# Kernel tuning notes

Hardware: AMD Instinct MI355X
Metric: run time of the kernel (lower is better)

The kernel has to match this reference:

```python
import jax, jax.numpy as jnp
import numpy as np

NUM_FEATURES = 512
NUM_HID = 16
NUM_CLASSES = 40


def _glorot(key, shape):
    lim = float(np.sqrt(6.0 / (shape[0] + shape[1])))
    return jax.random.uniform(key, shape, jnp.float32, -lim, lim)


def setup_inputs() -> dict:
    key = jax.random.key(0)
    k1, k2, k3, k4 = jax.random.split(key, 4)
    N, E = 100000, 3200000
    x = jax.random.normal(k1, (N, NUM_FEATURES), jnp.float32)
    edge_index = jax.random.randint(k2, (2, E), 0, N, jnp.int64)
    W1 = _glorot(k3, (NUM_FEATURES, NUM_HID))
    b1 = jnp.zeros((NUM_HID,), jnp.float32)
    W2 = _glorot(k4, (NUM_HID, NUM_CLASSES))
    b2 = jnp.zeros((NUM_CLASSES,), jnp.float32)
    return {"x": x, "edge_index": edge_index, "num_nodes": N,
            "W1": W1, "b1": b1, "W2": W2, "b2": b2}


def gcn_conv(x, src, dst, norm, W, b, num_nodes):
    # linear transform first (PyG GCNConv), then normalized scatter-add
    h = x @ W                                    # [N, out]
    msg = h[src] * norm[:, None]                 # [E+N, out]
    agg = jax.ops.segment_sum(msg, dst, num_segments=num_nodes)
    return agg + b


def reference(x, edge_index, num_nodes, W1, b1, W2, b2):
    # add self-loops and compute symmetric normalization deg^-1/2 A_hat deg^-1/2
    loops = jnp.arange(num_nodes, dtype=edge_index.dtype)
    src = jnp.concatenate([edge_index[0], loops])
    dst = jnp.concatenate([edge_index[1], loops])
    ones = jnp.ones(src.shape, x.dtype)
    deg = jax.ops.segment_sum(ones, dst, num_segments=num_nodes)
    dinv = jnp.where(deg > 0, deg ** -0.5, 0.0)
    norm = dinv[src] * dinv[dst]

    h = jax.nn.relu(gcn_conv(x, src, dst, norm, W1, b1, num_nodes))
    # dropout omitted: inference mode (training=False)
    h = gcn_conv(h, src, dst, norm, W2, b2, num_nodes)
    out = jax.nn.softmax(h, axis=1)
    return (out, h)
```

## Files before the change

### kernel.cpp

```cpp
#include <hip/hip_runtime.h>
#include <math.h>

#define F 512
#define H 16
#define C 40
#define BW 128
#define BSH 7
#define NB_MAX 1024
#define CHUNK 4096
#define EPT 16
#define SRC_BITS 17
#define SRC_MASK 0x1FFFF
#define SORT_CAP 8192

__global__ __launch_bounds__(256) void k_scatfuse(const int* __restrict__ src,
                                                  const int* __restrict__ dst,
                                                  int* __restrict__ gcnt,
                                                  int* __restrict__ ebuf, int E, int NB) {
    __shared__ int hist[NB_MAX];
    __shared__ int base2[NB_MAX];
    __shared__ int cur[NB_MAX];
    __shared__ int tsum[256];
    __shared__ int paddr[CHUNK];
    __shared__ int pdata[CHUNK];
    int c = blockIdx.x, t = threadIdx.x;
    int i0 = c * CHUNK;
    int nval = min(CHUNK, E - i0);
    for (int b = t; b < NB; b += 256) hist[b] = 0;
    int dreg[EPT], sreg[EPT];
    #pragma unroll
    for (int j = 0; j < EPT; j++) {
        int i = t + j * 256;
        if (i < nval) { dreg[j] = dst[i0 + i]; sreg[j] = src[i0 + i]; }
        else dreg[j] = -1;
    }
    __syncthreads();
    #pragma unroll
    for (int j = 0; j < EPT; j++)
        if (dreg[j] >= 0) atomicAdd(&hist[dreg[j] >> BSH], 1);
    __syncthreads();
    int b0 = t * 4;
    int v0 = (b0 + 0 < NB) ? hist[b0 + 0] : 0;
    int v1 = (b0 + 1 < NB) ? hist[b0 + 1] : 0;
    int v2 = (b0 + 2 < NB) ? hist[b0 + 2] : 0;
    int v3 = (b0 + 3 < NB) ? hist[b0 + 3] : 0;
    int loc1 = v0, loc2 = v0 + v1, loc3 = v0 + v1 + v2;
    int s = loc3 + v3;
    tsum[t] = s;
    __syncthreads();
    for (int off = 1; off < 256; off <<= 1) {
        int v = (t >= off) ? tsum[t - off] : 0;
        __syncthreads();
        tsum[t] += v;
        __syncthreads();
    }
    int excl = tsum[t] - s;
    if (b0 + 0 < NB) { int p = excl;        cur[b0+0] = p; int g = v0 ? atomicAdd(&gcnt[b0+0], v0) : 0; base2[b0+0] = (b0+0)*SORT_CAP + g - p; }
    if (b0 + 1 < NB) { int p = excl + loc1; cur[b0+1] = p; int g = v1 ? atomicAdd(&gcnt[b0+1], v1) : 0; base2[b0+1] = (b0+1)*SORT_CAP + g - p; }
    if (b0 + 2 < NB) { int p = excl + loc2; cur[b0+2] = p; int g = v2 ? atomicAdd(&gcnt[b0+2], v2) : 0; base2[b0+2] = (b0+2)*SORT_CAP + g - p; }
    if (b0 + 3 < NB) { int p = excl + loc3; cur[b0+3] = p; int g = v3 ? atomicAdd(&gcnt[b0+3], v3) : 0; base2[b0+3] = (b0+3)*SORT_CAP + g - p; }
    __syncthreads();
    #pragma unroll
    for (int j = 0; j < EPT; j++) {
        int d = dreg[j];
        if (d < 0) continue;
        int b = d >> BSH;
        int r = atomicAdd(&cur[b], 1);
        paddr[r] = base2[b] + r;
        pdata[r] = ((d & (BW - 1)) << SRC_BITS) | sreg[j];
    }
    __syncthreads();
    for (int i = t; i < nval; i += 256)
        ebuf[paddr[i]] = pdata[i];
}

__global__ __launch_bounds__(256) void k_sortb(int* __restrict__ ebuf,
                                               const int* __restrict__ gcnt,
                                               int* __restrict__ rowbeg,
                                               int* __restrict__ rowend,
                                               float* __restrict__ dinv, int N) {
    __shared__ int buf[SORT_CAP];
    __shared__ int hist[BW];
    __shared__ int off[BW];
    __shared__ int cur[BW];
    int b = blockIdx.x;
    int beg = b * SORT_CAP;
    int len = gcnt[b];
    if (len > SORT_CAP) len = SORT_CAP;
    int tid = threadIdx.x;
    if (tid < BW) hist[tid] = 0;
    for (int i = tid; i < len; i += 256) buf[i] = ebuf[beg + i];
    __syncthreads();
    for (int i = tid; i < len; i += 256)
        atomicAdd(&hist[buf[i] >> SRC_BITS], 1);
    __syncthreads();
    if (tid < BW) off[tid] = hist[tid];
    __syncthreads();
    for (int d = 1; d < BW; d <<= 1) {
        int v = (tid < BW && tid >= d) ? off[tid - d] : 0;
        __syncthreads();
        if (tid < BW) off[tid] += v;
        __syncthreads();
    }
    if (tid < BW) {
        int excl = off[tid] - hist[tid];
        int n = b * BW + tid;
        if (n < N) {
            rowbeg[n] = beg + excl;
            rowend[n] = beg + off[tid];
            dinv[n] = rsqrtf((float)(hist[tid] + 1));
        }
        cur[tid] = excl;
    }
    __syncthreads();
    for (int i = tid; i < len; i += 256) {
        int w = buf[i];
        int r = atomicAdd(&cur[w >> SRC_BITS], 1);
        ebuf[beg + r] = w & SRC_MASK;
    }
}

#define KT 64
#define GST 68
__global__ __launch_bounds__(64) void k_gemm1(const float* __restrict__ x,
                                              const float* __restrict__ W1,
                                              const float* __restrict__ dinv,
                                              float* __restrict__ h0s, int N) {
    __shared__ float xs[64 * GST];
    int t = threadIdx.x;
    int n0 = blockIdx.x * 64;
    float acc[H];
    #pragma unroll
    for (int j = 0; j < H; j++) acc[j] = 0.f;
    for (int kt = 0; kt < F; kt += KT) {
        __syncthreads();
        #pragma unroll
        for (int p = 0; p < 16; p++) {
            int idx = t + (p << 6);
            int r = idx >> 4, c4 = idx & 15;
            int v = n0 + r; if (v >= N) v = N - 1;
            float4 val = *(const float4*)(x + (size_t)v * F + kt + (c4 << 2));
            *(float4*)&xs[r * GST + (c4 << 2)] = val;
        }
        __syncthreads();
        #pragma unroll
        for (int k4 = 0; k4 < 16; k4++) {
            float4 xv = *(const float4*)&xs[t * GST + (k4 << 2)];
            const float* w = W1 + (size_t)(kt + (k4 << 2)) * H;
            #pragma unroll
            for (int j = 0; j < H; j++) acc[j] = fmaf(xv.x, w[j], acc[j]);
            #pragma unroll
            for (int j = 0; j < H; j++) acc[j] = fmaf(xv.y, w[H + j], acc[j]);
            #pragma unroll
            for (int j = 0; j < H; j++) acc[j] = fmaf(xv.z, w[2 * H + j], acc[j]);
            #pragma unroll
            for (int j = 0; j < H; j++) acc[j] = fmaf(xv.w, w[3 * H + j], acc[j]);
        }
    }
    int v = n0 + t;
    if (v >= N) return;
    float dv = dinv[v];
    float4* o4 = (float4*)(h0s + (size_t)v * H);
    o4[0] = make_float4(acc[0] * dv, acc[1] * dv, acc[2] * dv, acc[3] * dv);
    o4[1] = make_float4(acc[4] * dv, acc[5] * dv, acc[6] * dv, acc[7] * dv);
    o4[2] = make_float4(acc[8] * dv, acc[9] * dv, acc[10] * dv, acc[11] * dv);
    o4[3] = make_float4(acc[12] * dv, acc[13] * dv, acc[14] * dv, acc[15] * dv);
}

__global__ __launch_bounds__(256) void k_agg1(const float* __restrict__ hs,
                                              const int* __restrict__ adj,
                                              const int* __restrict__ rowbeg,
                                              const int* __restrict__ rowend,
                                              const float* __restrict__ dinv,
                                              const float* __restrict__ b1,
                                              float* __restrict__ out, int N) {
    int t = blockIdx.x * 256 + threadIdx.x;
    int n = t >> 2, q = t & 3;
    if (n >= N) return;
    const float4* hs4 = (const float4*)hs;
    int beg = rowbeg[n], end = rowend[n];
    float4 a = hs4[(size_t)n * 4 + q];
    float ax = a.x, ay = a.y, az = a.z, aw = a.w;
    int e = beg;
    for (; e + 7 < end; e += 8) {
        int s0 = adj[e], s1 = adj[e + 1], s2 = adj[e + 2], s3 = adj[e + 3];
        int s4 = adj[e + 4], s5 = adj[e + 5], s6 = adj[e + 6], s7 = adj[e + 7];
        float4 v0 = hs4[(size_t)s0 * 4 + q];
        float4 v1 = hs4[(size_t)s1 * 4 + q];
        float4 v2 = hs4[(size_t)s2 * 4 + q];
        float4 v3 = hs4[(size_t)s3 * 4 + q];
        float4 v4 = hs4[(size_t)s4 * 4 + q];
        float4 v5 = hs4[(size_t)s5 * 4 + q];
        float4 v6 = hs4[(size_t)s6 * 4 + q];
        float4 v7 = hs4[(size_t)s7 * 4 + q];
        ax += ((v0.x + v1.x) + (v2.x + v3.x)) + ((v4.x + v5.x) + (v6.x + v7.x));
        ay += ((v0.y + v1.y) + (v2.y + v3.y)) + ((v4.y + v5.y) + (v6.y + v7.y));
        az += ((v0.z + v1.z) + (v2.z + v3.z)) + ((v4.z + v5.z) + (v6.z + v7.z));
        aw += ((v0.w + v1.w) + (v2.w + v3.w)) + ((v4.w + v5.w) + (v6.w + v7.w));
    }
    for (; e + 3 < end; e += 4) {
        int s0 = adj[e], s1 = adj[e + 1], s2 = adj[e + 2], s3 = adj[e + 3];
        float4 v0 = hs4[(size_t)s0 * 4 + q];
        float4 v1 = hs4[(size_t)s1 * 4 + q];
        float4 v2 = hs4[(size_t)s2 * 4 + q];
        float4 v3 = hs4[(size_t)s3 * 4 + q];
        ax += (v0.x + v1.x) + (v2.x + v3.x);
        ay += (v0.y + v1.y) + (v2.y + v3.y);
        az += (v0.z + v1.z) + (v2.z + v3.z);
        aw += (v0.w + v1.w) + (v2.w + v3.w);
    }
    for (; e < end; e++) {
        int s = adj[e];
        float4 v = hs4[(size_t)s * 4 + q];
        ax += v.x; ay += v.y; az += v.z; aw += v.w;
    }
    float dv = dinv[n];
    float4 r;
    r.x = fmaxf(fmaf(dv, ax, b1[q * 4 + 0]), 0.f) * dv;
    r.y = fmaxf(fmaf(dv, ay, b1[q * 4 + 1]), 0.f) * dv;
    r.z = fmaxf(fmaf(dv, az, b1[q * 4 + 2]), 0.f) * dv;
    r.w = fmaxf(fmaf(dv, aw, b1[q * 4 + 3]), 0.f) * dv;
    ((float4*)out)[(size_t)n * 4 + q] = r;
}

__global__ __launch_bounds__(256) void k_agg2out(const float* __restrict__ hs,
                                                 const int* __restrict__ adj,
                                                 const int* __restrict__ rowbeg,
                                                 const int* __restrict__ rowend,
                                                 const float* __restrict__ dinv,
                                                 const float* __restrict__ W2,
                                                 const float* __restrict__ b2,
                                                 float* __restrict__ dout, int N) {
    __shared__ float sg[64 * 16];
    __shared__ float w2s[H * C];
    __shared__ float b2s[C];
    __shared__ float so[64 * 40];
    int t = threadIdx.x;
    for (int i = t; i < H * C; i += 256) w2s[i] = W2[i];
    if (t < C) b2s[t] = b2[t];
    int nl = t >> 2, q = t & 3;
    int n0 = blockIdx.x * 64;
    int n = n0 + nl;
    bool valid = (n < N);
    int nn = valid ? n : N - 1;
    const float4* hs4 = (const float4*)hs;
    int beg = rowbeg[nn], end = rowend[nn];
    float4 a = hs4[(size_t)nn * 4 + q];
    float ax = a.x, ay = a.y, az = a.z, aw = a.w;
    int e = beg;
    for (; e + 7 < end; e += 8) {
        int s0 = adj[e], s1 = adj[e + 1], s2 = adj[e + 2], s3 = adj[e + 3];
        int s4 = adj[e + 4], s5 = adj[e + 5], s6 = adj[e + 6], s7 = adj[e + 7];
        float4 v0 = hs4[(size_t)s0 * 4 + q];
        float4 v1 = hs4[(size_t)s1 * 4 + q];
        float4 v2 = hs4[(size_t)s2 * 4 + q];
        float4 v3 = hs4[(size_t)s3 * 4 + q];
        float4 v4 = hs4[(size_t)s4 * 4 + q];
        float4 v5 = hs4[(size_t)s5 * 4 + q];
        float4 v6 = hs4[(size_t)s6 * 4 + q];
        float4 v7 = hs4[(size_t)s7 * 4 + q];
        ax += ((v0.x + v1.x) + (v2.x + v3.x)) + ((v4.x + v5.x) + (v6.x + v7.x));
        ay += ((v0.y + v1.y) + (v2.y + v3.y)) + ((v4.y + v5.y) + (v6.y + v7.y));
        az += ((v0.z + v1.z) + (v2.z + v3.z)) + ((v4.z + v5.z) + (v6.z + v7.z));
        aw += ((v0.w + v1.w) + (v2.w + v3.w)) + ((v4.w + v5.w) + (v6.w + v7.w));
    }
    for (; e + 3 < end; e += 4) {
        int s0 = adj[e], s1 = adj[e + 1], s2 = adj[e + 2], s3 = adj[e + 3];
        float4 v0 = hs4[(size_t)s0 * 4 + q];
        float4 v1 = hs4[(size_t)s1 * 4 + q];
        float4 v2 = hs4[(size_t)s2 * 4 + q];
        float4 v3 = hs4[(size_t)s3 * 4 + q];
        ax += (v0.x + v1.x) + (v2.x + v3.x);
        ay += (v0.y + v1.y) + (v2.y + v3.y);
        az += (v0.z + v1.z) + (v2.z + v3.z);
        aw += (v0.w + v1.w) + (v2.w + v3.w);
    }
    for (; e < end; e++) {
        int s = adj[e];
        float4 v = hs4[(size_t)s * 4 + q];
        ax += v.x; ay += v.y; az += v.z; aw += v.w;
    }
    float dv = dinv[nn];
    *(float4*)&sg[nl * 16 + q * 4] = make_float4(dv * ax, dv * ay, dv * az, dv * aw);
    __syncthreads();
    float g16[16];
    #pragma unroll
    for (int k4 = 0; k4 < 4; k4++) {
        float4 gv = *(const float4*)&sg[nl * 16 + k4 * 4];
        g16[k4 * 4] = gv.x; g16[k4 * 4 + 1] = gv.y;
        g16[k4 * 4 + 2] = gv.z; g16[k4 * 4 + 3] = gv.w;
    }
    int j0 = q * 10;
    float h2[10];
    #pragma unroll
    for (int jj = 0; jj < 10; jj++) {
        float acc = b2s[j0 + jj];
        #pragma unroll
        for (int k = 0; k < H; k++) acc = fmaf(g16[k], w2s[k * C + j0 + jj], acc);
        h2[jj] = acc;
    }
    float m = h2[0];
    #pragma unroll
    for (int jj = 1; jj < 10; jj++) m = fmaxf(m, h2[jj]);
    m = fmaxf(m, __shfl_xor(m, 1, 64));
    m = fmaxf(m, __shfl_xor(m, 2, 64));
    float ex[10], ssum = 0.f;
    #pragma unroll
    for (int jj = 0; jj < 10; jj++) { ex[jj] = __expf(h2[jj] - m); ssum += ex[jj]; }
    ssum += __shfl_xor(ssum, 1, 64);
    ssum += __shfl_xor(ssum, 2, 64);
    float inv = 1.f / ssum;
    int rows = min(64, N - n0);
    int tot = rows * 10;
    #pragma unroll
    for (int jj = 0; jj < 10; jj++) so[nl * 40 + j0 + jj] = ex[jj] * inv;
    __syncthreads();
    {
        const float4* sp4 = (const float4*)so;
        float4* o4 = (float4*)(dout + (size_t)n0 * C);
        for (int i = t; i < tot; i += 256) o4[i] = sp4[i];
    }
    __syncthreads();
    #pragma unroll
    for (int jj = 0; jj < 10; jj++) so[nl * 40 + j0 + jj] = h2[jj];
    __syncthreads();
    {
        const float4* sp4 = (const float4*)so;
        float4* o4 = (float4*)(dout + (size_t)N * C + (size_t)n0 * C);
        for (int i = t; i < tot; i += 256) o4[i] = sp4[i];
    }
}

extern "C" void kernel_launch(void* const* d_in, const int* in_sizes, int n_in,
                              void* d_out, int out_size, void* d_ws, size_t ws_size,
                              hipStream_t stream) {
    const float* x  = (const float*)d_in[0];
    const int*   ei = (const int*)d_in[1];
    const float* W1 = (const float*)d_in[3];
    const float* b1 = (const float*)d_in[4];
    const float* W2 = (const float*)d_in[5];
    const float* b2 = (const float*)d_in[6];
    float* out = (float*)d_out;

    int N = in_sizes[0] / F;
    int E = in_sizes[1] / 2;
    const int* src = ei;
    const int* dst = ei + E;
    int NB  = (N + BW - 1) / BW;
    int NCH = (E + CHUNK - 1) / CHUNK;

    float* ws = (float*)d_ws;
    size_t o = 0;
    int* gcnt   = (int*)(ws + o); o += (size_t)NB_MAX;
    int* rowbeg = (int*)(ws + o); o += (size_t)N + 4;
    int* rowend = (int*)(ws + o); o += (size_t)N + 4;
    int* ebuf   = (int*)(ws + o); o += (size_t)NB * SORT_CAP + CHUNK;
    float* dinv = ws + o;         o += (size_t)N;
    float* h0s  = ws + o;         o += (size_t)N * H;
    float* h1s  = ws + o;         o += (size_t)N * H;

    int ng = (N + 63) / 64;

    hipMemsetAsync(gcnt, 0, (size_t)NB * sizeof(int), stream);
    k_scatfuse<<<NCH, 256, 0, stream>>>(src, dst, gcnt, ebuf, E, NB);
    k_sortb   <<<NB, 256, 0, stream>>>(ebuf, gcnt, rowbeg, rowend, dinv, N);
    k_gemm1   <<<ng, 64, 0, stream>>>(x, W1, dinv, h0s, N);
    k_agg1    <<<(N * 4 + 255) / 256, 256, 0, stream>>>(h0s, ebuf, rowbeg, rowend, dinv, b1, h1s, N);
    k_agg2out <<<ng, 256, 0, stream>>>(h1s, ebuf, rowbeg, rowend, dinv, W2, b2, out, N);
}
```

Before: 541.1 us.

## Drop per-row sort; aggregate bucketed edges with shared-memory atomics

Removes the per-bucket counting-sort kernel and the rowbeg/rowend CSR arrays. Degrees are now counted with global atomics in the scatter kernel. Both aggregation kernels now process one 128-node bucket per block, accumulating messages into shared memory with float atomics on the packed (local dst, src) edge words. Edge loads in the scatter kernel are vectorised to int4. This trades a sort pass and its extra memory traffic for shared-memory atomic contention, a 3.2M-op global atomic degree count, and fewer, larger blocks (782) for the aggregations.

```diff
diff --git a/kernel.cpp b/kernel.cpp
--- a/kernel.cpp
+++ b/kernel.cpp
@@ -12,10 +12,12 @@
 #define SRC_BITS 17
 #define SRC_MASK 0x1FFFF
 #define SORT_CAP 8192
+#define AST 17
 
 __global__ __launch_bounds__(256) void k_scatfuse(const int* __restrict__ src,
                                                   const int* __restrict__ dst,
                                                   int* __restrict__ gcnt,
+                                                  int* __restrict__ deg,
                                                   int* __restrict__ ebuf, int E, int NB) {
     __shared__ int hist[NB_MAX];
     __shared__ int base2[NB_MAX];
@@ -27,17 +29,33 @@
     int i0 = c * CHUNK;
     int nval = min(CHUNK, E - i0);
     for (int b = t; b < NB; b += 256) hist[b] = 0;
+    const int4* s4 = (const int4*)(src + i0);
+    const int4* d4 = (const int4*)(dst + i0);
     int dreg[EPT], sreg[EPT];
     #pragma unroll
-    for (int j = 0; j < EPT; j++) {
-        int i = t + j * 256;
-        if (i < nval) { dreg[j] = dst[i0 + i]; sreg[j] = src[i0 + i]; }
-        else dreg[j] = -1;
+    for (int j = 0; j < EPT / 4; j++) {
+        int i4 = t + j * 256;
+        int base = i4 * 4;
+        if (base + 3 < nval) {
+            int4 dv = d4[i4], sv = s4[i4];
+            dreg[j*4+0] = dv.x; dreg[j*4+1] = dv.y; dreg[j*4+2] = dv.z; dreg[j*4+3] = dv.w;
+            sreg[j*4+0] = sv.x; sreg[j*4+1] = sv.y; sreg[j*4+2] = sv.z; sreg[j*4+3] = sv.w;
+        } else {
+            #pragma unroll
+            for (int k = 0; k < 4; k++) {
+                int idx = base + k;
+                if (idx < nval) { dreg[j*4+k] = dst[i0 + idx]; sreg[j*4+k] = src[i0 + idx]; }
+                else dreg[j*4+k] = -1;
+            }
+        }
     }
     __syncthreads();
     #pragma unroll
     for (int j = 0; j < EPT; j++)
-        if (dreg[j] >= 0) atomicAdd(&hist[dreg[j] >> BSH], 1);
+        if (dreg[j] >= 0) {
+            atomicAdd(&hist[dreg[j] >> BSH], 1);
+            atomicAdd(&deg[dreg[j]], 1);
+        }
     __syncthreads();
     int b0 = t * 4;
     int v0 = (b0 + 0 < NB) ? hist[b0 + 0] : 0;
@@ -74,57 +92,11 @@
         ebuf[paddr[i]] = pdata[i];
 }
 
-__global__ __launch_bounds__(256) void k_sortb(int* __restrict__ ebuf,
-                                               const int* __restrict__ gcnt,
-                                               int* __restrict__ rowbeg,
-                                               int* __restrict__ rowend,
-                                               float* __restrict__ dinv, int N) {
-    __shared__ int buf[SORT_CAP];
-    __shared__ int hist[BW];
-    __shared__ int off[BW];
-    __shared__ int cur[BW];
-    int b = blockIdx.x;
-    int beg = b * SORT_CAP;
-    int len = gcnt[b];
-    if (len > SORT_CAP) len = SORT_CAP;
-    int tid = threadIdx.x;
-    if (tid < BW) hist[tid] = 0;
-    for (int i = tid; i < len; i += 256) buf[i] = ebuf[beg + i];
-    __syncthreads();
-    for (int i = tid; i < len; i += 256)
-        atomicAdd(&hist[buf[i] >> SRC_BITS], 1);
-    __syncthreads();
-    if (tid < BW) off[tid] = hist[tid];
-    __syncthreads();
-    for (int d = 1; d < BW; d <<= 1) {
-        int v = (tid < BW && tid >= d) ? off[tid - d] : 0;
-        __syncthreads();
-        if (tid < BW) off[tid] += v;
-        __syncthreads();
-    }
-    if (tid < BW) {
-        int excl = off[tid] - hist[tid];
-        int n = b * BW + tid;
-        if (n < N) {
-            rowbeg[n] = beg + excl;
-            rowend[n] = beg + off[tid];
-            dinv[n] = rsqrtf((float)(hist[tid] + 1));
-        }
-        cur[tid] = excl;
-    }
-    __syncthreads();
-    for (int i = tid; i < len; i += 256) {
-        int w = buf[i];
-        int r = atomicAdd(&cur[w >> SRC_BITS], 1);
-        ebuf[beg + r] = w & SRC_MASK;
-    }
-}
-
 #define KT 64
 #define GST 68
 __global__ __launch_bounds__(64) void k_gemm1(const float* __restrict__ x,
                                               const float* __restrict__ W1,
-                                              const float* __restrict__ dinv,
+                                              const int* __restrict__ deg,
                                               float* __restrict__ h0s, int N) {
     __shared__ float xs[64 * GST];
     int t = threadIdx.x;
@@ -159,7 +131,7 @@
     }
     int v = n0 + t;
     if (v >= N) return;
-    float dv = dinv[v];
+    float dv = rsqrtf((float)deg[v] + 1.0f);
     float4* o4 = (float4*)(h0s + (size_t)v * H);
     o4[0] = make_float4(acc[0] * dv, acc[1] * dv, acc[2] * dv, acc[3] * dv);
     o4[1] = make_float4(acc[4] * dv, acc[5] * dv, acc[6] * dv, acc[7] * dv);
@@ -167,166 +139,156 @@
     o4[3] = make_float4(acc[12] * dv, acc[13] * dv, acc[14] * dv, acc[15] * dv);
 }
 
-__global__ __launch_bounds__(256) void k_agg1(const float* __restrict__ hs,
-                                              const int* __restrict__ adj,
-                                              const int* __restrict__ rowbeg,
-                                              const int* __restrict__ rowend,
-                                              const float* __restrict__ dinv,
-                                              const float* __restrict__ b1,
-                                              float* __restrict__ out, int N) {
-    int t = blockIdx.x * 256 + threadIdx.x;
-    int n = t >> 2, q = t & 3;
+__global__ __launch_bounds__(256) void k_agg1b(const float* __restrict__ hs,
+                                               const int* __restrict__ ebuf,
+                                               const int* __restrict__ gcnt,
+                                               const int* __restrict__ deg,
+                                               const float* __restrict__ b1,
+                                               float* __restrict__ out, int N) {
+    __shared__ float acc[BW * AST];
+    int b = blockIdx.x, t = threadIdx.x;
+    for (int i = t; i < BW * AST; i += 256) acc[i] = 0.f;
+    int beg = b * SORT_CAP;
+    int len = min(gcnt[b], SORT_CAP);
+    __syncthreads();
+    int q = t & 3, eq = t >> 2;
+    const float4* hs4 = (const float4*)hs;
+    const int4* e4 = (const int4*)(ebuf + beg);
+    int nfull = len >> 2;
+    for (int i = eq; i < nfull; i += 64) {
+        int4 w4 = e4[i];
+        #pragma unroll
+        for (int k = 0; k < 4; k++) {
+            int w = (k == 0) ? w4.x : (k == 1) ? w4.y : (k == 2) ? w4.z : w4.w;
+            int dl = w >> SRC_BITS, s = w & SRC_MASK;
+            float4 v = hs4[(size_t)s * 4 + q];
+            float* ap = &acc[dl * AST + q * 4];
+            atomicAdd(&ap[0], v.x);
+            atomicAdd(&ap[1], v.y);
+            atomicAdd(&ap[2], v.z);
+            atomicAdd(&ap[3], v.w);
+        }
+    }
+    for (int e = (nfull << 2) + eq; e < len; e += 64) {
+        int w = ebuf[beg + e];
+        int dl = w >> SRC_BITS, s = w & SRC_MASK;
+        float4 v = hs4[(size_t)s * 4 + q];
+        float* ap = &acc[dl * AST + q * 4];
+        atomicAdd(&ap[0], v.x);
+        atomicAdd(&ap[1], v.y);
+        atomicAdd(&ap[2], v.z);
+        atomicAdd(&ap[3], v.w);
+    }
+    __syncthreads();
+    int nl = t >> 1, half = t & 1;
+    int n = b * BW + nl;
     if (n >= N) return;
-    const float4* hs4 = (const float4*)hs;
-    int beg = rowbeg[n], end = rowend[n];
-    float4 a = hs4[(size_t)n * 4 + q];
-    float ax = a.x, ay = a.y, az = a.z, aw = a.w;
-    int e = beg;
-    for (; e + 7 < end; e += 8) {
-        int s0 = adj[e], s1 = adj[e + 1], s2 = adj[e + 2], s3 = adj[e + 3];
-        int s4 = adj[e + 4], s5 = adj[e + 5], s6 = adj[e + 6], s7 = adj[e + 7];
-        float4 v0 = hs4[(size_t)s0 * 4 + q];
-        float4 v1 = hs4[(size_t)s1 * 4 + q];
-        float4 v2 = hs4[(size_t)s2 * 4 + q];
-        float4 v3 = hs4[(size_t)s3 * 4 + q];
-        float4 v4 = hs4[(size_t)s4 * 4 + q];
-        float4 v5 = hs4[(size_t)s5 * 4 + q];
-        float4 v6 = hs4[(size_t)s6 * 4 + q];
-        float4 v7 = hs4[(size_t)s7 * 4 + q];
-        ax += ((v0.x + v1.x) + (v2.x + v3.x)) + ((v4.x + v5.x) + (v6.x + v7.x));
-        ay += ((v0.y + v1.y) + (v2.y + v3.y)) + ((v4.y + v5.y) + (v6.y + v7.y));
-        az += ((v0.z + v1.z) + (v2.z + v3.z)) + ((v4.z + v5.z) + (v6.z + v7.z));
-        aw += ((v0.w + v1.w) + (v2.w + v3.w)) + ((v4.w + v5.w) + (v6.w + v7.w));
-    }
-    for (; e + 3 < end; e += 4) {
-        int s0 = adj[e], s1 = adj[e + 1], s2 = adj[e + 2], s3 = adj[e + 3];
-        float4 v0 = hs4[(size_t)s0 * 4 + q];
-        float4 v1 = hs4[(size_t)s1 * 4 + q];
-        float4 v2 = hs4[(size_t)s2 * 4 + q];
-        float4 v3 = hs4[(size_t)s3 * 4 + q];
-        ax += (v0.x + v1.x) + (v2.x + v3.x);
-        ay += (v0.y + v1.y) + (v2.y + v3.y);
-        az += (v0.z + v1.z) + (v2.z + v3.z);
-        aw += (v0.w + v1.w) + (v2.w + v3.w);
-    }
-    for (; e < end; e++) {
-        int s = adj[e];
-        float4 v = hs4[(size_t)s * 4 + q];
-        ax += v.x; ay += v.y; az += v.z; aw += v.w;
-    }
-    float dv = dinv[n];
-    float4 r;
-    r.x = fmaxf(fmaf(dv, ax, b1[q * 4 + 0]), 0.f) * dv;
-    r.y = fmaxf(fmaf(dv, ay, b1[q * 4 + 1]), 0.f) * dv;
-    r.z = fmaxf(fmaf(dv, az, b1[q * 4 + 2]), 0.f) * dv;
-    r.w = fmaxf(fmaf(dv, aw, b1[q * 4 + 3]), 0.f) * dv;
-    ((float4*)out)[(size_t)n * 4 + q] = r;
-}
-
-__global__ __launch_bounds__(256) void k_agg2out(const float* __restrict__ hs,
-                                                 const int* __restrict__ adj,
-                                                 const int* __restrict__ rowbeg,
-                                                 const int* __restrict__ rowend,
-                                                 const float* __restrict__ dinv,
-                                                 const float* __restrict__ W2,
-                                                 const float* __restrict__ b2,
-                                                 float* __restrict__ dout, int N) {
-    __shared__ float sg[64 * 16];
+    float dv = rsqrtf((float)deg[n] + 1.0f);
+    int f0 = half * 8;
+    const float* selfp = hs + (size_t)n * H + f0;
+    const float* accp = &acc[nl * AST + f0];
+    float o[8];
+    #pragma unroll
+    for (int j = 0; j < 8; j++) {
+        float a = accp[j] + selfp[j];
+        o[j] = fmaxf(fmaf(dv, a, b1[f0 + j]), 0.f) * dv;
+    }
+    float4* d4 = (float4*)(out + (size_t)n * H + f0);
+    d4[0] = make_float4(o[0], o[1], o[2], o[3]);
+    d4[1] = make_float4(o[4], o[5], o[6], o[7]);
+}
+
+__global__ __launch_bounds__(256) void k_agg2b(const float* __restrict__ hs,
+                                               const int* __restrict__ ebuf,
+                                               const int* __restrict__ gcnt,
+                                               const int* __restrict__ deg,
+                                               const float* __restrict__ W2,
+                                               const float* __restrict__ b2,
+                                               float* __restrict__ dout, int N) {
+    __shared__ float acc[BW * AST];
     __shared__ float w2s[H * C];
     __shared__ float b2s[C];
-    __shared__ float so[64 * 40];
-    int t = threadIdx.x;
+    __shared__ float so[BW * C];
+    int b = blockIdx.x, t = threadIdx.x;
     for (int i = t; i < H * C; i += 256) w2s[i] = W2[i];
     if (t < C) b2s[t] = b2[t];
-    int nl = t >> 2, q = t & 3;
-    int n0 = blockIdx.x * 64;
-    int n = n0 + nl;
+    for (int i = t; i < BW * AST; i += 256) acc[i] = 0.f;
+    int beg = b * SORT_CAP;
+    int len = min(gcnt[b], SORT_CAP);
+    __syncthreads();
+    int q = t & 3, eq = t >> 2;
+    const float4* hs4 = (const float4*)hs;
+    const int4* e4 = (const int4*)(ebuf + beg);
+    int nfull = len >> 2;
+    for (int i = eq; i < nfull; i += 64) {
+        int4 w4 = e4[i];
+        #pragma unroll
+        for (int k = 0; k < 4; k++) {
+            int w = (k == 0) ? w4.x : (k == 1) ? w4.y : (k == 2) ? w4.z : w4.w;
+            int dl = w >> SRC_BITS, s = w & SRC_MASK;
+            float4 v = hs4[(size_t)s * 4 + q];
+            float* ap = &acc[dl * AST + q * 4];
+            atomicAdd(&ap[0], v.x);
+            atomicAdd(&ap[1], v.y);
+            atomicAdd(&ap[2], v.z);
+            atomicAdd(&ap[3], v.w);
+        }
+    }
+    for (int e = (nfull << 2) + eq; e < len; e += 64) {
+        int w = ebuf[beg + e];
+        int dl = w >> SRC_BITS, s = w & SRC_MASK;
+        float4 v = hs4[(size_t)s * 4 + q];
+        float* ap = &acc[dl * AST + q * 4];
+        atomicAdd(&ap[0], v.x);
+        atomicAdd(&ap[1], v.y);
+        atomicAdd(&ap[2], v.z);
+        atomicAdd(&ap[3], v.w);
+    }
+    __syncthreads();
+    int nl = t >> 1, half = t & 1;
+    int n = b * BW + nl;
     bool valid = (n < N);
     int nn = valid ? n : N - 1;
-    const float4* hs4 = (const float4*)hs;
-    int beg = rowbeg[nn], end = rowend[nn];
-    float4 a = hs4[(size_t)nn * 4 + q];
-    float ax = a.x, ay = a.y, az = a.z, aw = a.w;
-    int e = beg;
-    for (; e + 7 < end; e += 8) {
-        int s0 = adj[e], s1 = adj[e + 1], s2 = adj[e + 2], s3 = adj[e + 3];
-        int s4 = adj[e + 4], s5 = adj[e + 5], s6 = adj[e + 6], s7 = adj[e + 7];
-        float4 v0 = hs4[(size_t)s0 * 4 + q];
-        float4 v1 = hs4[(size_t)s1 * 4 + q];
-        float4 v2 = hs4[(size_t)s2 * 4 + q];
-        float4 v3 = hs4[(size_t)s3 * 4 + q];
-        float4 v4 = hs4[(size_t)s4 * 4 + q];
-        float4 v5 = hs4[(size_t)s5 * 4 + q];
-        float4 v6 = hs4[(size_t)s6 * 4 + q];
-        float4 v7 = hs4[(size_t)s7 * 4 + q];
-        ax += ((v0.x + v1.x) + (v2.x + v3.x)) + ((v4.x + v5.x) + (v6.x + v7.x));
-        ay += ((v0.y + v1.y) + (v2.y + v3.y)) + ((v4.y + v5.y) + (v6.y + v7.y));
-        az += ((v0.z + v1.z) + (v2.z + v3.z)) + ((v4.z + v5.z) + (v6.z + v7.z));
-        aw += ((v0.w + v1.w) + (v2.w + v3.w)) + ((v4.w + v5.w) + (v6.w + v7.w));
-    }
-    for (; e + 3 < end; e += 4) {
-        int s0 = adj[e], s1 = adj[e + 1], s2 = adj[e + 2], s3 = adj[e + 3];
-        float4 v0 = hs4[(size_t)s0 * 4 + q];
-        float4 v1 = hs4[(size_t)s1 * 4 + q];
-        float4 v2 = hs4[(size_t)s2 * 4 + q];
-        float4 v3 = hs4[(size_t)s3 * 4 + q];
-        ax += (v0.x + v1.x) + (v2.x + v3.x);
-        ay += (v0.y + v1.y) + (v2.y + v3.y);
-        az += (v0.z + v1.z) + (v2.z + v3.z);
-        aw += (v0.w + v1.w) + (v2.w + v3.w);
-    }
-    for (; e < end; e++) {
-        int s = adj[e];
-        float4 v = hs4[(size_t)s * 4 + q];
-        ax += v.x; ay += v.y; az += v.z; aw += v.w;
-    }
-    float dv = dinv[nn];
-    *(float4*)&sg[nl * 16 + q * 4] = make_float4(dv * ax, dv * ay, dv * az, dv * aw);
-    __syncthreads();
-    float g16[16];
-    #pragma unroll
-    for (int k4 = 0; k4 < 4; k4++) {
-        float4 gv = *(const float4*)&sg[nl * 16 + k4 * 4];
-        g16[k4 * 4] = gv.x; g16[k4 * 4 + 1] = gv.y;
-        g16[k4 * 4 + 2] = gv.z; g16[k4 * 4 + 3] = gv.w;
-    }
-    int j0 = q * 10;
-    float h2[10];
-    #pragma unroll
-    for (int jj = 0; jj < 10; jj++) {
-        float acc = b2s[j0 + jj];
-        #pragma unroll
-        for (int k = 0; k < H; k++) acc = fmaf(g16[k], w2s[k * C + j0 + jj], acc);
-        h2[jj] = acc;
+    float dv = rsqrtf((float)deg[nn] + 1.0f);
+    float g[H];
+    #pragma unroll
+    for (int k = 0; k < H; k++)
+        g[k] = dv * (acc[nl * AST + k] + hs[(size_t)nn * H + k]);
+    int j0 = half * 20;
+    float h2[20];
+    #pragma unroll
+    for (int jj = 0; jj < 20; jj++) {
+        float a = b2s[j0 + jj];
+        #pragma unroll
+        for (int k = 0; k < H; k++) a = fmaf(g[k], w2s[k * C + j0 + jj], a);
+        h2[jj] = a;
     }
     float m = h2[0];
     #pragma unroll
-    for (int jj = 1; jj < 10; jj++) m = fmaxf(m, h2[jj]);
+    for (int jj = 1; jj < 20; jj++) m = fmaxf(m, h2[jj]);
     m = fmaxf(m, __shfl_xor(m, 1, 64));
-    m = fmaxf(m, __shfl_xor(m, 2, 64));
-    float ex[10], ssum = 0.f;
-    #pragma unroll
-    for (int jj = 0; jj < 10; jj++) { ex[jj] = __expf(h2[jj] - m); ssum += ex[jj]; }
+    float ex[20], ssum = 0.f;
+    #pragma unroll
+    for (int jj = 0; jj < 20; jj++) { ex[jj] = __expf(h2[jj] - m); ssum += ex[jj]; }
     ssum += __shfl_xor(ssum, 1, 64);
-    ssum += __shfl_xor(ssum, 2, 64);
     float inv = 1.f / ssum;
-    int rows = min(64, N - n0);
-    int tot = rows * 10;
-    #pragma unroll
-    for (int jj = 0; jj < 10; jj++) so[nl * 40 + j0 + jj] = ex[jj] * inv;
+    int rows = min(BW, N - b * BW);
+    int tot = rows * (C / 4);
+    #pragma unroll
+    for (int jj = 0; jj < 20; jj++) so[nl * C + j0 + jj] = ex[jj] * inv;
     __syncthreads();
     {
         const float4* sp4 = (const float4*)so;
-        float4* o4 = (float4*)(dout + (size_t)n0 * C);
+        float4* o4 = (float4*)(dout + (size_t)b * BW * C);
         for (int i = t; i < tot; i += 256) o4[i] = sp4[i];
     }
     __syncthreads();
     #pragma unroll
-    for (int jj = 0; jj < 10; jj++) so[nl * 40 + j0 + jj] = h2[jj];
+    for (int jj = 0; jj < 20; jj++) so[nl * C + j0 + jj] = h2[jj];
     __syncthreads();
     {
         const float4* sp4 = (const float4*)so;
-        float4* o4 = (float4*)(dout + (size_t)N * C + (size_t)n0 * C);
+        float4* o4 = (float4*)(dout + (size_t)N * C + (size_t)b * BW * C);
         for (int i = t; i < tot; i += 256) o4[i] = sp4[i];
     }
 }
@@ -351,20 +313,18 @@
 
     float* ws = (float*)d_ws;
     size_t o = 0;
-    int* gcnt   = (int*)(ws + o); o += (size_t)NB_MAX;
-    int* rowbeg = (int*)(ws + o); o += (size_t)N + 4;
-    int* rowend = (int*)(ws + o); o += (size_t)N + 4;
-    int* ebuf   = (int*)(ws + o); o += (size_t)NB * SORT_CAP + CHUNK;
-    float* dinv = ws + o;         o += (size_t)N;
-    float* h0s  = ws + o;         o += (size_t)N * H;
-    float* h1s  = ws + o;         o += (size_t)N * H;
+    int* gcnt = (int*)(ws + o); o += (size_t)NB_MAX;
+    int* deg  = (int*)(ws + o); o += (size_t)N;
+    o = (o + 3) & ~(size_t)3;
+    int* ebuf = (int*)(ws + o); o += (size_t)NB * SORT_CAP + CHUNK;
+    float* h0s = ws + o;        o += (size_t)N * H;
+    float* h1s = ws + o;        o += (size_t)N * H;
 
     int ng = (N + 63) / 64;
 
-    hipMemsetAsync(gcnt, 0, (size_t)NB * sizeof(int), stream);
-    k_scatfuse<<<NCH, 256, 0, stream>>>(src, dst, gcnt, ebuf, E, NB);
-    k_sortb   <<<NB, 256, 0, stream>>>(ebuf, gcnt, rowbeg, rowend, dinv, N);
-    k_gemm1   <<<ng, 64, 0, stream>>>(x, W1, dinv, h0s, N);
-    k_agg1    <<<(N * 4 + 255) / 256, 256, 0, stream>>>(h0s, ebuf, rowbeg, rowend, dinv, b1, h1s, N);
-    k_agg2out <<<ng, 256, 0, stream>>>(h1s, ebuf, rowbeg, rowend, dinv, W2, b2, out, N);
-}
+    hipMemsetAsync(gcnt, 0, ((size_t)NB_MAX + N) * sizeof(int), stream);
+    k_scatfuse<<<NCH, 256, 0, stream>>>(src, dst, gcnt, deg, ebuf, E, NB);
+    k_gemm1   <<<ng, 64, 0, stream>>>(x, W1, deg, h0s, N);
+    k_agg1b   <<<NB, 256, 0, stream>>>(h0s, ebuf, gcnt, deg, b1, h1s, N);
+    k_agg2b   <<<NB, 256, 0, stream>>>(h1s, ebuf, gcnt, deg, W2, b2, out, N);
+}
```

Measured after the change: 1.202 ms. 2.22x slower.
